# Kernel optimization log

Hardware: AMD Instinct MI355X
Metric: run time of the kernel (lower is better)

## Reference

```python
import jax, jax.numpy as jnp
import numpy as np

B, N, D = 4, 4096, 512          # batch, seq_len, hidden_size
H, DH = 8, 64                    # n_heads, head_dim
M = 512                          # nb_features = 0.125 * seq_len
LN_EPS = 1e-12
KERNEL_EPS = 1e-4


def setup_inputs() -> dict:
    key = jax.random.key(0)
    ks = jax.random.split(key, 12)
    s = 0.02
    return {
        "input_tensor": jax.random.normal(ks[0], (B, N, D), jnp.float32),
        "attention_mask": jnp.zeros((B, 1, 1, N), jnp.float32),  # unused by module
        "Wq": jax.random.normal(ks[1], (D, D), jnp.float32) * s,
        "bq": jnp.zeros((D,), jnp.float32),
        "Wk": jax.random.normal(ks[2], (D, D), jnp.float32) * s,
        "bk": jnp.zeros((D,), jnp.float32),
        "Wv": jax.random.normal(ks[3], (D, D), jnp.float32) * s,
        "bv": jnp.zeros((D,), jnp.float32),
        # gaussian (orthogonal-style) random feature projections [M, DH]
        "proj_q": jax.random.normal(ks[4], (M, DH), jnp.float32),
        "proj_k": jax.random.normal(ks[5], (M, DH), jnp.float32),
        "Wd": jax.random.normal(ks[6], (D, D), jnp.float32) * s,
        "bd": jnp.zeros((D,), jnp.float32),
        "gamma": jnp.ones((D,), jnp.float32),
        "beta": jnp.zeros((D,), jnp.float32),
    }


def _softmax_kernel(data, projection_matrix, is_query):
    # data: [B,H,N,DH], projection_matrix: [M,DH]
    data_normalizer = data.shape[-1] ** (-0.25)
    ratio = projection_matrix.shape[0] ** (-0.5)
    data_dash = jnp.einsum("bhnd,md->bhnm", data_normalizer * data, projection_matrix)
    diag_data = (jnp.sum(data * data, axis=-1) * 0.5 * data_normalizer ** 2)[..., None]
    if is_query:
        stab = jnp.max(data_dash, axis=-1, keepdims=True)
    else:
        stab = jnp.max(data_dash)  # global max, per original code
    return ratio * (jnp.exp(data_dash - diag_data - stab) + KERNEL_EPS)


def _linear_attention(q, k, v):
    # q,k: [B,H,N,M]; v: [B,H,N,DH]
    k_cumsum = jnp.sum(k, axis=-2)                               # [B,H,M]
    d_inv = 1.0 / jnp.einsum("bhnm,bhm->bhn", q, k_cumsum)       # [B,H,N]
    context = jnp.einsum("bhnm,bhne->bhme", k, v)                # [B,H,M,DH]
    return jnp.einsum("bhme,bhnm,bhn->bhne", context, q, d_inv)  # [B,H,N,DH]


def reference(input_tensor, attention_mask, Wq, bq, Wk, bk, Wv, bv,
              proj_q, proj_k, Wd, bd, gamma, beta):
    def heads(x):  # [B,N,D] -> [B,H,N,DH]
        return x.reshape(B, N, H, DH).transpose(0, 2, 1, 3)

    q = heads(input_tensor @ Wq.T + bq)
    k = heads(input_tensor @ Wk.T + bk)
    v = heads(input_tensor @ Wv.T + bv)

    q = _softmax_kernel(q, proj_q, is_query=True)
    k = _softmax_kernel(k, proj_k, is_query=False)

    ctx = _linear_attention(q, k, v)                  # [B,H,N,DH]
    ctx = ctx.transpose(0, 2, 1, 3).reshape(B, N, D)  # merge heads

    hidden = ctx @ Wd.T + bd                          # dropout is identity (eval)
    x = hidden + input_tensor
    mu = jnp.mean(x, axis=-1, keepdims=True)
    var = jnp.mean((x - mu) ** 2, axis=-1, keepdims=True)
    return (x - mu) / jnp.sqrt(var + LN_EPS) * gamma + beta
```

## Files before the change

### kernel.cpp

```cpp
#include <hip/hip_runtime.h>
#include <math.h>

typedef __bf16 bf16;
typedef __bf16 bf16x8 __attribute__((ext_vector_type(8)));
typedef __bf16 bf16x4 __attribute__((ext_vector_type(4)));
typedef float  f32x4  __attribute__((ext_vector_type(4)));

#define NSEQ 4096
#define DMODEL 512
#define DHEAD 64
#define MFEAT 512
#define BHEADS 32
#define ROWS_TOTAL 16384

#define NORMALIZER 0.35355339059327373f
#define DIAG_C 0.0625f
#define KEPS 1e-4f

__device__ __forceinline__ float warpReduceSum(float v) {
#pragma unroll
    for (int off = 32; off > 0; off >>= 1) v += __shfl_xor(v, off);
    return v;
}

__device__ __forceinline__ void atomicMaxF(float* addr, float val) {
    int* ai = (int*)addr;
    int cur = __float_as_int(*addr);
    while (__int_as_float(cur) < val) {
        int prev = atomicCAS(ai, cur, __float_as_int(val));
        if (prev == cur) break;
        cur = prev;
    }
}

__device__ __forceinline__ void gload16(const void* g, void* l) {
    __builtin_amdgcn_global_load_lds((const __attribute__((address_space(1))) void*)g,
                                     (__attribute__((address_space(3))) void*)l, 16, 0, 0);
}

__global__ __launch_bounds__(256)
void prep_convert(const float* __restrict__ x, const float* __restrict__ Wq,
                  const float* __restrict__ Wk, const float* __restrict__ Wv,
                  const float* __restrict__ Wd, const float* __restrict__ pq,
                  const float* __restrict__ bq, const float* __restrict__ bk,
                  const float* __restrict__ bv,
                  bf16* __restrict__ xb, bf16* __restrict__ Wb,
                  bf16* __restrict__ Wdb, bf16* __restrict__ pqb,
                  float* __restrict__ bcat)
{
    size_t i4 = (size_t)blockIdx.x * 256 + threadIdx.x;
    size_t e0 = i4 * 4;
    if (e0 >= 9471488) return;
    const float* src;
    if (e0 < 8388608) {
        src = x + e0;
        float4 v = *(const float4*)src;
        bf16* d = xb + e0;
        d[0] = (bf16)v.x; d[1] = (bf16)v.y; d[2] = (bf16)v.z; d[3] = (bf16)v.w;
    } else if (e0 < 9175040) {
        size_t c = e0 - 8388608; int wsel = (int)(c >> 18); size_t o = c & 262143;
        src = (wsel == 0 ? Wq : wsel == 1 ? Wk : Wv) + o;
        float4 v = *(const float4*)src;
        bf16* d = Wb + c;
        d[0] = (bf16)v.x; d[1] = (bf16)v.y; d[2] = (bf16)v.z; d[3] = (bf16)v.w;
    } else if (e0 < 9437184) {
        size_t c = e0 - 9175040;
        src = Wd + c;
        float4 v = *(const float4*)src;
        bf16* d = Wdb + c;
        d[0] = (bf16)v.x; d[1] = (bf16)v.y; d[2] = (bf16)v.z; d[3] = (bf16)v.w;
    } else if (e0 < 9469952) {
        size_t c = e0 - 9437184;
        src = pq + c;
        float4 v = *(const float4*)src;
        const int feat = (int)(c >> 6), col = (int)(c & 63);
        bf16x4 d4;
        d4[0] = (bf16)v.x; d4[1] = (bf16)v.y; d4[2] = (bf16)v.z; d4[3] = (bf16)v.w;
        const int inrow = (col << 1) ^ ((feat & 7) << 4);
        *(bf16x4*)((char*)pqb + (size_t)feat * 128 + inrow) = d4;
    } else {
        size_t c = e0 - 9469952; int wsel = (int)(c >> 9); size_t o = c & 511;
        src = (wsel == 0 ? bq : wsel == 1 ? bk : bv) + o;
        *(float4*)(bcat + c) = *(const float4*)src;
    }
}

template<int MODE>
__global__ __launch_bounds__(256)
void gemm_mfma(const bf16* __restrict__ A, const bf16* __restrict__ Bw,
               const float* __restrict__ bias, const float* __restrict__ resid,
               bf16* __restrict__ outQ, bf16* __restrict__ outK,
               bf16* __restrict__ outV, float* __restrict__ outF)
{
    __shared__ char As[16384];
    __shared__ char Bs[16384];
    const int tid = threadIdx.x;
    const int w = tid >> 6, l = tid & 63;
    const int wr = w >> 1, wc = w & 1;
    const int row0 = blockIdx.y << 7;
    const int col0 = blockIdx.x << 7;

    f32x4 acc[4][4] = {};
    const char* Ab = (const char*)A + (size_t)row0 * 1024;
    const char* Bb = (const char*)Bw + (size_t)col0 * 1024;

    for (int kt = 0; kt < 8; ++kt) {
        const int k0b = kt << 7;
#pragma unroll
        for (int i = 0; i < 4; ++i) {
            int off = (i << 12) + (tid << 4);
            int g = off ^ ((off >> 3) & 0x70);
            int grow = g >> 7, gcol = g & 127;
            gload16(Ab + (size_t)grow * 1024 + k0b + gcol, As + (i << 12) + (w << 10));
            gload16(Bb + (size_t)grow * 1024 + k0b + gcol, Bs + (i << 12) + (w << 10));
        }
        __syncthreads();
#pragma unroll
        for (int ks = 0; ks < 2; ++ks) {
            bf16x8 af[4], bb[4];
#pragma unroll
            for (int mi = 0; mi < 4; ++mi) {
                int row = (wr << 6) + (mi << 4) + (l & 15);
                int addr = ((row << 7) + (ks << 6) + ((l >> 4) << 4)) ^ ((row & 7) << 4);
                af[mi] = *(const bf16x8*)(As + addr);
            }
#pragma unroll
            for (int nj = 0; nj < 4; ++nj) {
                int row = (wc << 6) + (nj << 4) + (l & 15);
                int addr = ((row << 7) + (ks << 6) + ((l >> 4) << 4)) ^ ((row & 7) << 4);
                bb[nj] = *(const bf16x8*)(Bs + addr);
            }
#pragma unroll
            for (int mi = 0; mi < 4; ++mi)
#pragma unroll
                for (int nj = 0; nj < 4; ++nj)
                    acc[mi][nj] = __builtin_amdgcn_mfma_f32_16x16x32_bf16(af[mi], bb[nj], acc[mi][nj], 0, 0, 0);
        }
        __syncthreads();
    }

    const int subrow = (l >> 4) << 2;
    const int subcol = l & 15;
#pragma unroll
    for (int mi = 0; mi < 4; ++mi) {
#pragma unroll
        for (int nj = 0; nj < 4; ++nj) {
            const int cg = col0 + (wc << 6) + (nj << 4) + subcol;
            const float bi = bias[cg];
            const int rgb = row0 + (wr << 6) + (mi << 4) + subrow;
            if (MODE == 0) {
                if (cg < 512) {
                    const int hh = cg >> 6, ee = cg & 63;
                    const int bb2 = rgb >> 12, n = rgb & 4095;
#pragma unroll
                    for (int r = 0; r < 4; ++r)
                        outQ[((size_t)((bb2 * 8 + hh) * 4096 + n + r)) * 64 + ee] =
                            (bf16)(acc[mi][nj][r] + bi);
                } else if (cg < 1024) {
                    const int eg = cg - 512, hh = eg >> 6, ee = eg & 63;
#pragma unroll
                    for (int r = 0; r < 4; ++r) {
                        const int rg = rgb + r;
                        *(bf16*)((char*)outK + (size_t)rg * 1024 + hh * 128 +
                                 ((ee * 2) ^ ((rg & 7) << 4))) = (bf16)(acc[mi][nj][r] + bi);
                    }
                } else {
                    const int eg = cg - 1024, hh = eg >> 6, ee = eg & 63;
                    const int bb2 = rgb >> 12, n = rgb & 4095;
                    bf16x4 pv;
#pragma unroll
                    for (int r = 0; r < 4; ++r) pv[r] = (bf16)(acc[mi][nj][r] + bi);
                    const int nb = n * 2;
                    size_t byteaddr = (size_t)((bb2 * 8 + hh) * 64 + ee) * 8192
                                    + (size_t)((nb & ~127) | ((nb & 127) ^ ((ee & 7) << 4)));
                    *(bf16x4*)((char*)outV + byteaddr) = pv;
                }
            } else {
#pragma unroll
                for (int r = 0; r < 4; ++r) {
                    const int rg = rgb + r;
                    outF[(size_t)rg * 512 + cg] = acc[mi][nj][r] + bi + resid[(size_t)rg * 512 + cg];
                }
            }
        }
    }
}

__global__ __launch_bounds__(64)
void vsum_kernel(const bf16* __restrict__ Vt, float* __restrict__ vsum)
{
    const int row = blockIdx.x;
    const bf16x8* p = (const bf16x8*)((const char*)Vt + (size_t)row * 8192);
    float s = 0.f;
#pragma unroll
    for (int i = 0; i < 8; ++i) {
        bf16x8 v = p[threadIdx.x + i * 64];
#pragma unroll
        for (int u = 0; u < 8; ++u) s += (float)v[u];
    }
    s = warpReduceSum(s);
    if (threadIdx.x == 0) vsum[row] = s;
}

__global__ __launch_bounds__(256)
void diag_kernel(const bf16* __restrict__ Kb, float* __restrict__ dgk)
{
    const int idx = blockIdx.x * 256 + threadIdx.x;
    const int bh = idx >> 12, n = idx & 4095;
    const int b = bh >> 3, h = bh & 7;
    const char* row = (const char*)Kb + (size_t)(b * 4096 + n) * 1024 + h * 128;
    const int sw = (n & 7) << 4;
    float ss = 0.f;
#pragma unroll
    for (int j = 0; j < 8; ++j) {
        bf16x8 v = *(const bf16x8*)(row + ((j << 4) ^ sw));
#pragma unroll
        for (int u = 0; u < 8; ++u) { float f = (float)v[u]; ss += f * f; }
    }
    dgk[idx] = DIAG_C * ss;
}

__global__ __launch_bounds__(256, 2)
void kside_mfma7(const bf16* __restrict__ Kb, const bf16* __restrict__ Vt,
                 const float* __restrict__ projk, const float* __restrict__ dgk,
                 float* __restrict__ ctxp8, float* __restrict__ esumf8,
                 float* __restrict__ gmax)
{
    __shared__ char K_s[16384];
    __shared__ char V_s[16384];
    __shared__ char E_s[32768];

    const int tid = threadIdx.x;
    const int w = tid >> 6, l = tid & 63;
    const int lq = l & 15, lg = l >> 4;
    const int bh = blockIdx.x;
    const int b = bh >> 3, h = bh & 7;
    const int mw = (blockIdx.y << 8) + (w << 6);
    const int z = blockIdx.z;
    const int swl = (lq & 7) << 4;

    bf16x8 pk[4][2];
#pragma unroll
    for (int mj = 0; mj < 4; ++mj)
#pragma unroll
        for (int ks = 0; ks < 2; ++ks) {
            const int m = mw + (mj << 4) + lq;
            const float* p = projk + (size_t)m * 64 + (ks << 5) + (lg << 3);
            float4 a = *(const float4*)p;
            float4 c = *(const float4*)(p + 4);
            bf16x8 f;
            f[0] = (bf16)(NORMALIZER * a.x); f[1] = (bf16)(NORMALIZER * a.y);
            f[2] = (bf16)(NORMALIZER * a.z); f[3] = (bf16)(NORMALIZER * a.w);
            f[4] = (bf16)(NORMALIZER * c.x); f[5] = (bf16)(NORMALIZER * c.y);
            f[6] = (bf16)(NORMALIZER * c.z); f[7] = (bf16)(NORMALIZER * c.w);
            pk[mj][ks] = f;
        }

    const char* kgb = (const char*)Kb + (size_t)(b * 4096) * 1024 + h * 128;
    const char* vgb = (const char*)Vt + (size_t)bh * 64 * 8192;
    const float* dgb = dgk + (bh << 12) + (z << 9);
    char* tw = E_s + (w << 13);
    const f32x4 Zc = {0.f, 0.f, 0.f, 0.f};

    f32x4 acc2[4][4] = {};
    float esacc[4] = {0.f, 0.f, 0.f, 0.f};
    float lmax = -1e30f;

    {
        const int nc = z << 9;
#pragma unroll
        for (int i = 0; i < 2; ++i) {
            const int lin = tid + (i << 8);
            const int row = lin >> 3, seg = (lin & 7) << 4;
            gload16(kgb + (size_t)(nc + row) * 1024 + seg, K_s + (lin << 4));
            gload16(vgb + (size_t)row * 8192 + (nc << 1) + seg, V_s + (lin << 4));
        }
    }

    int cur = 0;
    for (int c = 0; c < 8; ++c) {
        __syncthreads();
        if (c < 7) {
            const int nn = (z << 9) + ((c + 1) << 6);
#pragma unroll
            for (int i = 0; i < 2; ++i) {
                const int lin = tid + (i << 8);
                const int row = lin >> 3, seg = (lin & 7) << 4;
                gload16(kgb + (size_t)(nn + row) * 1024 + seg,
                        K_s + ((cur ^ 1) << 13) + (lin << 4));
                gload16(vgb + (size_t)row * 8192 + (nn << 1) + seg,
                        V_s + ((cur ^ 1) << 13) + (lin << 4));
            }
        }
        const char* Kc = K_s + (cur << 13);
        const char* Vc = V_s + (cur << 13);

#pragma unroll
        for (int nt = 0; nt < 4; ++nt) {
            const char* kr = Kc + (((nt << 4) + lq) << 7);
            bf16x8 a0 = *(const bf16x8*)(kr + ((lg << 4) ^ swl));
            bf16x8 a1 = *(const bf16x8*)(kr + ((64 + (lg << 4)) ^ swl));
            f32x4 acc1[4];
#pragma unroll
            for (int mj = 0; mj < 4; ++mj) {
                acc1[mj] = __builtin_amdgcn_mfma_f32_16x16x32_bf16(a0, pk[mj][0], Zc, 0, 0, 0);
                acc1[mj] = __builtin_amdgcn_mfma_f32_16x16x32_bf16(a1, pk[mj][1], acc1[mj], 0, 0, 0);
            }
            float4 dv = *(const float4*)(dgb + (c << 6) + (nt << 4) + (lg << 2));
            const float dgr[4] = {dv.x, dv.y, dv.z, dv.w};
#pragma unroll
            for (int mj = 0; mj < 4; ++mj) {
                bf16x4 ev;
#pragma unroll
                for (int r = 0; r < 4; ++r) {
                    const float d = acc1[mj][r];
                    lmax = fmaxf(lmax, d);
                    const float e = __expf(d - dgr[r]);
                    esacc[mj] += e;
                    ev[r] = (bf16)e;
                }
                *(bf16x4*)(tw + (((mj << 4) + lq) << 7) +
                           (((nt << 5) + (lg << 3)) ^ swl)) = ev;
            }
        }
#pragma unroll
        for (int ks2 = 0; ks2 < 2; ++ks2) {
            bf16x8 be[4];
#pragma unroll
            for (int mj = 0; mj < 4; ++mj)
                be[mj] = *(const bf16x8*)(tw + (((mj << 4) + lq) << 7) +
                                          (((ks2 << 6) + (lg << 4)) ^ swl));
#pragma unroll
            for (int et = 0; et < 4; ++et) {
                const int e = (et << 4) + lq;
                bf16x8 av = *(const bf16x8*)(Vc + (e << 7) +
                                             (((ks2 << 6) + (lg << 4)) ^ swl));
#pragma unroll
                for (int mj = 0; mj < 4; ++mj)
                    acc2[et][mj] = __builtin_amdgcn_mfma_f32_16x16x32_bf16(av, be[mj], acc2[et][mj], 0, 0, 0);
            }
        }
        cur ^= 1;
    }

#pragma unroll
    for (int mj = 0; mj < 4; ++mj) {
        float s = esacc[mj];
        s += __shfl_xor(s, 16); s += __shfl_xor(s, 32);
        if (l < 16)
            esumf8[((size_t)z * 32 + bh) * 512 + mw + (mj << 4) + lq] = s;
    }
#pragma unroll
    for (int off = 32; off > 0; off >>= 1) lmax = fmaxf(lmax, __shfl_xor(lmax, off));
    if (l == 0) atomicMaxF(gmax, lmax);

    float* cz = ctxp8 + (size_t)z * (32 * 64 * 512) + (size_t)bh * 64 * 512;
#pragma unroll
    for (int et = 0; et < 4; ++et)
#pragma unroll
        for (int mj = 0; mj < 4; ++mj)
#pragma unroll
            for (int r = 0; r < 4; ++r) {
                const int e = (et << 4) + (lg << 2) + r;
                cz[(size_t)e * 512 + mw + (mj << 4) + lq] = acc2[et][mj][r];
            }
}

__global__ __launch_bounds__(256)
void finalize_ctx(const float* __restrict__ ctxp8, const float* __restrict__ esumf8,
                  bf16* __restrict__ ctxE, float* __restrict__ ctxsum,
                  float* __restrict__ esumsum)
{
    __shared__ float red_s[4][64];
    const int tid = threadIdx.x;
    const int bh = blockIdx.x;
    const int mc = blockIdx.y << 7;
    const int e = tid & 63, ms = tid >> 6;
    const size_t Z = (size_t)32 * 64 * 512;

    const float* cb = ctxp8 + (size_t)bh * 64 * 512 + (size_t)e * 512 + mc + (ms << 5);
    char* obr = (char*)ctxE + ((size_t)bh * 80 + e) * 1024;
    float s = 0.f;
#pragma unroll
    for (int i8 = 0; i8 < 4; ++i8) {
        float acc[8] = {};
#pragma unroll
        for (int zz = 0; zz < 8; ++zz) {
            float4 v0 = *(const float4*)(cb + zz * Z + (i8 << 3));
            float4 v1 = *(const float4*)(cb + zz * Z + (i8 << 3) + 4);
            acc[0] += v0.x; acc[1] += v0.y; acc[2] += v0.z; acc[3] += v0.w;
            acc[4] += v1.x; acc[5] += v1.y; acc[6] += v1.z; acc[7] += v1.w;
        }
        bf16x8 p8;
#pragma unroll
        for (int u = 0; u < 8; ++u) { s += acc[u]; p8[u] = (bf16)acc[u]; }
        const int mloc = mc + (ms << 5) + (i8 << 3);
        *(bf16x8*)(obr + ((mloc << 1) ^ ((e & 7) << 4))) = p8;
    }
    red_s[ms][e] = s;
    __syncthreads();
    if (tid < 64)
        atomicAdd(ctxsum + bh * 64 + tid,
                  red_s[0][tid] + red_s[1][tid] + red_s[2][tid] + red_s[3][tid]);
    if (tid < 128) {
        const int m = mc + tid;
        float ev = 0.f;
#pragma unroll
        for (int zz = 0; zz < 8; ++zz)
            ev += esumf8[((size_t)zz * 32 + bh) * 512 + m];
        bf16* er = ctxE + (size_t)(bh * 80 + 64) * 512;
        er[m] = (bf16)1.0f;
        er[512 + (m ^ 8)] = (bf16)ev;
        float t = warpReduceSum(ev);
        if ((tid & 63) == 0) atomicAdd(esumsum + bh, t);
    }
}

__global__ __launch_bounds__(512, 1)
void qside_mfma4(const bf16* __restrict__ Qb, const bf16* __restrict__ Pq,
                 const bf16* __restrict__ CtxE, const float* __restrict__ vsum,
                 const float* __restrict__ ctxsum, const float* __restrict__ esumsum,
                 const float* __restrict__ gmax, bf16* __restrict__ OutC)
{
    __shared__ char ctx_s[81920];
    __shared__ char pq_s[2][16384];
    __shared__ char T_s[40960];

    const int tid = threadIdx.x;
    const int w = tid >> 6, l = tid & 63;
    const int lq = l & 15, lg = l >> 4;
    const int bh = blockIdx.x;
    const int b = bh >> 3, h = bh & 7;
    const int n0 = blockIdx.y << 9;

    const char* ctxg = (const char*)CtxE + (size_t)bh * 81920;
    const char* pqg  = (const char*)Pq;
#pragma unroll
    for (int i = 0; i < 10; ++i)
        gload16(ctxg + (i << 13) + (tid << 4), ctx_s + (i << 13) + (w << 10));
#pragma unroll
    for (int p = 0; p < 2; ++p)
        gload16(pqg + (p << 13) + (tid << 4), pq_s[0] + (p << 13) + (w << 10));

    const char* qgb = (const char*)Qb + ((size_t)bh * 4096 + n0 + (w << 6)) * 128;
    bf16x8 qa[4][2];
    float diag_l[4];
#pragma unroll
    for (int ni = 0; ni < 4; ++ni) {
        const char* qr = qgb + ((ni << 4) + lq) * 128;
        float ss = 0.f;
#pragma unroll
        for (int kk = 0; kk < 2; ++kk) {
            qa[ni][kk] = *(const bf16x8*)(qr + (kk << 6) + (lg << 4));
#pragma unroll
            for (int u = 0; u < 8; ++u) { float f = (float)qa[ni][kk][u]; ss += f * f; }
        }
        ss += __shfl_xor(ss, 16);
        ss += __shfl_xor(ss, 32);
        diag_l[ni] = DIAG_C * ss;
    }

    f32x4 acc2[4][5] = {};
    float mmax[4] = {-1e30f, -1e30f, -1e30f, -1e30f};
    char* tw = T_s + w * 5120;
    const f32x4 Zc = {0.f, 0.f, 0.f, 0.f};

    __syncthreads();

    for (int ft = 0; ft < 4; ++ft) {
        const int buf = ft & 1;
        if (ft < 3) {
#pragma unroll
            for (int p = 0; p < 2; ++p)
                gload16(pqg + ((ft + 1) << 14) + (p << 13) + (tid << 4),
                        pq_s[buf ^ 1] + (p << 13) + (w << 10));
        }
        const char* pqb = pq_s[buf];
#pragma unroll
        for (int sl = 0; sl < 4; ++sl) {
            f32x4 acc1[2][4];
#pragma unroll
            for (int mi = 0; mi < 2; ++mi) {
                const int fr = (sl << 5) + (mi << 4) + lq;
                bf16x8 pf = *(const bf16x8*)(pqb + fr * 128 +
                              (((lg << 4)) ^ ((lq & 7) << 4)));
#pragma unroll
                for (int ni = 0; ni < 4; ++ni)
                    acc1[mi][ni] = __builtin_amdgcn_mfma_f32_16x16x32_bf16(pf, qa[ni][0], Zc, 0, 0, 0);
            }
#pragma unroll
            for (int mi = 0; mi < 2; ++mi) {
                const int fr = (sl << 5) + (mi << 4) + lq;
                bf16x8 pf = *(const bf16x8*)(pqb + fr * 128 +
                              ((64 + (lg << 4)) ^ ((lq & 7) << 4)));
#pragma unroll
                for (int ni = 0; ni < 4; ++ni)
                    acc1[mi][ni] = __builtin_amdgcn_mfma_f32_16x16x32_bf16(pf, qa[ni][1], acc1[mi][ni], 0, 0, 0);
            }
#pragma unroll
            for (int mi = 0; mi < 2; ++mi)
#pragma unroll
                for (int ni = 0; ni < 4; ++ni) {
                    bf16x4 tv;
#pragma unroll
                    for (int r = 0; r < 4; ++r) {
                        const float qd = acc1[mi][ni][r];
                        mmax[ni] = fmaxf(mmax[ni], qd);
                        tv[r] = (bf16)__expf(NORMALIZER * qd - diag_l[ni]);
                    }
                    *(bf16x4*)(tw + ((ni << 4) + lq) * 80 + (mi << 5) + (lg << 3)) = tv;
                }
            bf16x8 ta[4];
#pragma unroll
            for (int ni = 0; ni < 4; ++ni)
                ta[ni] = *(const bf16x8*)(tw + ((ni << 4) + lq) * 80 + (lg << 4));
#pragma unroll
            for (int nj = 0; nj < 5; ++nj) {
                const int e = (nj << 4) + lq;
                bf16x8 cb = *(const bf16x8*)(ctx_s + e * 1024 +
                              (((ft << 8) + (sl << 6) + (lg << 4)) ^ ((e & 7) << 4)));
#pragma unroll
                for (int ni = 0; ni < 4; ++ni)
                    acc2[ni][nj] = __builtin_amdgcn_mfma_f32_16x16x32_bf16(ta[ni], cb, acc2[ni][nj], 0, 0, 0);
            }
        }
        __syncthreads();
    }

    const float sG = __expf(-gmax[0]);
    const float ess = esumsum[bh];
    bf16* outb = OutC + ((size_t)(b * 4096) + n0 + (w << 6)) * 512 + (h << 6);
#pragma unroll
    for (int ni = 0; ni < 4; ++ni) {
        float mmr = mmax[ni];
        mmr = fmaxf(mmr, __shfl_xor(mmr, 16));
        mmr = fmaxf(mmr, __shfl_xor(mmr, 32));
#pragma unroll
        for (int r = 0; r < 4; ++r) {
            const float mm = __shfl(mmr, (lg << 2) + r);
            const float uT = __shfl(acc2[ni][4][r], (lg << 4));
            const float uE = __shfl(acc2[ni][4][r], (lg << 4) | 1);
            const float cr = __expf(-NORMALIZER * mm);
            const float qsum = cr * uT + KEPS * 512.0f;
            const float D = sG * (cr * uE + KEPS * ess) + KEPS * 4096.0f * qsum;
            const float inv = 1.0f / D;
            const float al = sG * cr * inv;
            const float G1 = sG * KEPS * inv;
            const float G2 = KEPS * qsum * inv;
            const int row = (ni << 4) + (lg << 2) + r;
#pragma unroll
            for (int nj = 0; nj < 4; ++nj) {
                const int e = (nj << 4) + lq;
                float v = al * acc2[ni][nj][r] + G1 * ctxsum[(bh << 6) + e] + G2 * vsum[(bh << 6) + e];
                outb[(size_t)row * 512 + e] = (bf16)v;
            }
        }
    }
}

__global__ __launch_bounds__(256)
void ln_kernel(const float* __restrict__ hid, const float* __restrict__ gamma,
               const float* __restrict__ beta, float* __restrict__ out)
{
    const int row = (blockIdx.x << 2) + (threadIdx.x >> 6);
    const int lane = threadIdx.x & 63;
    const float* x = hid + (size_t)row * DMODEL + (lane << 3);
    float4 a = *(const float4*)x;
    float4 c = *(const float4*)(x + 4);
    float s = a.x + a.y + a.z + a.w + c.x + c.y + c.z + c.w;
    float sq = a.x * a.x + a.y * a.y + a.z * a.z + a.w * a.w +
               c.x * c.x + c.y * c.y + c.z * c.z + c.w * c.w;
    s = warpReduceSum(s);
    sq = warpReduceSum(sq);
    const float mu = s * 0.001953125f;
    const float var = sq * 0.001953125f - mu * mu;
    const float rs = rsqrtf(var + 1e-12f);
    const float4 g1 = *(const float4*)(gamma + (lane << 3));
    const float4 g2 = *(const float4*)(gamma + (lane << 3) + 4);
    const float4 b1 = *(const float4*)(beta + (lane << 3));
    const float4 b2 = *(const float4*)(beta + (lane << 3) + 4);
    float4 o1, o2;
    o1.x = (a.x - mu) * rs * g1.x + b1.x;
    o1.y = (a.y - mu) * rs * g1.y + b1.y;
    o1.z = (a.z - mu) * rs * g1.z + b1.z;
    o1.w = (a.w - mu) * rs * g1.w + b1.w;
    o2.x = (c.x - mu) * rs * g2.x + b2.x;
    o2.y = (c.y - mu) * rs * g2.y + b2.y;
    o2.z = (c.z - mu) * rs * g2.z + b2.z;
    o2.w = (c.w - mu) * rs * g2.w + b2.w;
    *(float4*)(out + (size_t)row * DMODEL + (lane << 3)) = o1;
    *(float4*)(out + (size_t)row * DMODEL + (lane << 3) + 4) = o2;
}

__global__ void init_misc(float* gmax)
{
    if (threadIdx.x == 0 && blockIdx.x == 0) *gmax = -1e30f;
}

extern "C" void kernel_launch(void* const* d_in, const int* in_sizes, int n_in,
                              void* d_out, int out_size, void* d_ws, size_t ws_size,
                              hipStream_t stream)
{
    const float* x     = (const float*)d_in[0];
    const float* Wq    = (const float*)d_in[2];
    const float* bq    = (const float*)d_in[3];
    const float* Wk    = (const float*)d_in[4];
    const float* bk    = (const float*)d_in[5];
    const float* Wv    = (const float*)d_in[6];
    const float* bv    = (const float*)d_in[7];
    const float* projq = (const float*)d_in[8];
    const float* projk = (const float*)d_in[9];
    const float* Wd    = (const float*)d_in[10];
    const float* bd    = (const float*)d_in[11];
    const float* gamma = (const float*)d_in[12];
    const float* beta  = (const float*)d_in[13];

    char* W = (char*)d_ws;
    bf16*  qb16   = (bf16*) (W);
    bf16*  kb16s  = (bf16*) (W + 16777216);
    bf16*  vtb    = (bf16*) (W + 33554432);
    bf16*  xb16   = (bf16*) (W + 50331648);
    float* hidf32 = (float*)(W + 67108864);
    float* ctxp8  = (float*)(W + 67108864);
    float* esumf8 = (float*)(W + 100663296);
    float* dgk    = (float*)(W + 101187584);
    bf16*  Wb16   = (bf16*) (W + 100663296);
    bf16*  Wdb16  = (bf16*) (W + 102236160);
    bf16*  pqb16  = (bf16*) (W + 102760448);
    float* bcat   = (float*)(W + 102825984);
    bf16*  ctxE   = (bf16*) (W + 102832128);
    float* vsumb  = (float*)(W + 105453568);
    float* ctxsum = (float*)(W + 105461760);
    float* esmsm  = (float*)(W + 105469952);
    float* gmaxb  = (float*)(W + 105470080);

    prep_convert<<<9250, 256, 0, stream>>>(x, Wq, Wk, Wv, Wd, projq, bq, bk, bv,
                                           xb16, Wb16, Wdb16, pqb16, bcat);
    hipMemsetAsync(ctxE, 0, 2621440, stream);
    hipMemsetAsync(ctxsum, 0, 8192 + 128, stream);
    init_misc<<<1, 64, 0, stream>>>(gmaxb);

    gemm_mfma<0><<<dim3(12, 128), 256, 0, stream>>>(xb16, Wb16, bcat, nullptr,
                                                    qb16, kb16s, vtb, nullptr);

    diag_kernel<<<512, 256, 0, stream>>>(kb16s, dgk);
    vsum_kernel<<<2048, 64, 0, stream>>>(vtb, vsumb);
    kside_mfma7<<<dim3(32, 2, 8), 256, 0, stream>>>(kb16s, vtb, projk, dgk,
                                                    ctxp8, esumf8, gmaxb);
    finalize_ctx<<<dim3(32, 4), 256, 0, stream>>>(ctxp8, esumf8, ctxE, ctxsum, esmsm);

    qside_mfma4<<<dim3(32, 8), 512, 0, stream>>>(qb16, pqb16, ctxE, vsumb,
                                                 ctxsum, esmsm, gmaxb, xb16);

    gemm_mfma<1><<<dim3(4, 128), 256, 0, stream>>>(xb16, Wdb16, bd, x,
                                                   nullptr, nullptr, nullptr, hidf32);
    ln_kernel<<<4096, 256, 0, stream>>>(hidf32, gamma, beta, (float*)d_out);
}
```

Before: 201.8 us.

## Store K head-major and fuse feature halves into one 512-thread kside block

The QKV GEMM epilogue now writes K in a per-(batch,head) contiguous swizzled layout instead of token-major interleaved heads. This makes K chunk loads one contiguous 8KB block, and diag_kernel addresses rows linearly. The kside kernel now uses 512 threads covering all 512 features in one block, so K and exp tiles are no longer computed twice across blockIdx.y. The whole 64KB V slab for a z-chunk is preloaded once instead of double-buffered, which cuts redundant K loads and projections but raises LDS use to about 144KB and allows only one block per CU.

```diff
diff --git a/kernel.cpp b/kernel.cpp
--- a/kernel.cpp
+++ b/kernel.cpp
@@ -158,11 +158,12 @@
                             (bf16)(acc[mi][nj][r] + bi);
                 } else if (cg < 1024) {
                     const int eg = cg - 512, hh = eg >> 6, ee = eg & 63;
+                    const int bb2 = rgb >> 12;
 #pragma unroll
                     for (int r = 0; r < 4; ++r) {
-                        const int rg = rgb + r;
-                        *(bf16*)((char*)outK + (size_t)rg * 1024 + hh * 128 +
-                                 ((ee * 2) ^ ((rg & 7) << 4))) = (bf16)(acc[mi][nj][r] + bi);
+                        const int nn = (rgb & 4095) + r;
+                        *(bf16*)((char*)outK + ((size_t)(bb2 * 8 + hh) * 4096 + nn) * 128 +
+                                 ((ee * 2) ^ ((nn & 7) << 4))) = (bf16)(acc[mi][nj][r] + bi);
                     }
                 } else {
                     const int eg = cg - 1024, hh = eg >> 6, ee = eg & 63;
@@ -206,9 +207,8 @@
 void diag_kernel(const bf16* __restrict__ Kb, float* __restrict__ dgk)
 {
     const int idx = blockIdx.x * 256 + threadIdx.x;
-    const int bh = idx >> 12, n = idx & 4095;
-    const int b = bh >> 3, h = bh & 7;
-    const char* row = (const char*)Kb + (size_t)(b * 4096 + n) * 1024 + h * 128;
+    const int n = idx & 4095;
+    const char* row = (const char*)Kb + (size_t)idx * 128;
     const int sw = (n & 7) << 4;
     float ss = 0.f;
 #pragma unroll
@@ -220,23 +220,22 @@
     dgk[idx] = DIAG_C * ss;
 }
 
-__global__ __launch_bounds__(256, 2)
-void kside_mfma7(const bf16* __restrict__ Kb, const bf16* __restrict__ Vt,
+__global__ __launch_bounds__(512, 1)
+void kside_mfma8(const bf16* __restrict__ Kb, const bf16* __restrict__ Vt,
                  const float* __restrict__ projk, const float* __restrict__ dgk,
                  float* __restrict__ ctxp8, float* __restrict__ esumf8,
                  float* __restrict__ gmax)
 {
+    __shared__ char V_s[65536];
     __shared__ char K_s[16384];
-    __shared__ char V_s[16384];
-    __shared__ char E_s[32768];
+    __shared__ char E_s[65536];
 
     const int tid = threadIdx.x;
     const int w = tid >> 6, l = tid & 63;
     const int lq = l & 15, lg = l >> 4;
     const int bh = blockIdx.x;
-    const int b = bh >> 3, h = bh & 7;
-    const int mw = (blockIdx.y << 8) + (w << 6);
-    const int z = blockIdx.z;
+    const int z = blockIdx.y;
+    const int mw = w << 6;
     const int swl = (lq & 7) << 4;
 
     bf16x8 pk[4][2];
@@ -256,44 +255,29 @@
             pk[mj][ks] = f;
         }
 
-    const char* kgb = (const char*)Kb + (size_t)(b * 4096) * 1024 + h * 128;
-    const char* vgb = (const char*)Vt + (size_t)bh * 64 * 8192;
+    const char* kgb = (const char*)Kb + (size_t)bh * 524288 + (size_t)(z << 9) * 128;
+    const char* vgb = (const char*)Vt + (size_t)bh * 524288;
     const float* dgb = dgk + (bh << 12) + (z << 9);
     char* tw = E_s + (w << 13);
     const f32x4 Zc = {0.f, 0.f, 0.f, 0.f};
 
+#pragma unroll
+    for (int i = 0; i < 8; ++i)
+        gload16(vgb + (size_t)((i << 3) + w) * 8192 + (z << 10) + ((tid & 63) << 4),
+                V_s + (i << 13) + (tid << 4));
+    gload16(kgb + (tid << 4), K_s + (tid << 4));
+
     f32x4 acc2[4][4] = {};
     float esacc[4] = {0.f, 0.f, 0.f, 0.f};
     float lmax = -1e30f;
 
-    {
-        const int nc = z << 9;
-#pragma unroll
-        for (int i = 0; i < 2; ++i) {
-            const int lin = tid + (i << 8);
-            const int row = lin >> 3, seg = (lin & 7) << 4;
-            gload16(kgb + (size_t)(nc + row) * 1024 + seg, K_s + (lin << 4));
-            gload16(vgb + (size_t)row * 8192 + (nc << 1) + seg, V_s + (lin << 4));
-        }
-    }
-
     int cur = 0;
     for (int c = 0; c < 8; ++c) {
         __syncthreads();
-        if (c < 7) {
-            const int nn = (z << 9) + ((c + 1) << 6);
-#pragma unroll
-            for (int i = 0; i < 2; ++i) {
-                const int lin = tid + (i << 8);
-                const int row = lin >> 3, seg = (lin & 7) << 4;
-                gload16(kgb + (size_t)(nn + row) * 1024 + seg,
-                        K_s + ((cur ^ 1) << 13) + (lin << 4));
-                gload16(vgb + (size_t)row * 8192 + (nn << 1) + seg,
-                        V_s + ((cur ^ 1) << 13) + (lin << 4));
-            }
-        }
+        if (c < 7)
+            gload16(kgb + (size_t)((c + 1) << 13) + (tid << 4),
+                    K_s + ((cur ^ 1) << 13) + (tid << 4));
         const char* Kc = K_s + (cur << 13);
-        const char* Vc = V_s + (cur << 13);
 
 #pragma unroll
         for (int nt = 0; nt < 4; ++nt) {
@@ -333,7 +317,7 @@
 #pragma unroll
             for (int et = 0; et < 4; ++et) {
                 const int e = (et << 4) + lq;
-                bf16x8 av = *(const bf16x8*)(Vc + (e << 7) +
+                bf16x8 av = *(const bf16x8*)(V_s + (e << 10) + (c << 7) +
                                              (((ks2 << 6) + (lg << 4)) ^ swl));
 #pragma unroll
                 for (int mj = 0; mj < 4; ++mj)
@@ -645,8 +629,8 @@
 
     diag_kernel<<<512, 256, 0, stream>>>(kb16s, dgk);
     vsum_kernel<<<2048, 64, 0, stream>>>(vtb, vsumb);
-    kside_mfma7<<<dim3(32, 2, 8), 256, 0, stream>>>(kb16s, vtb, projk, dgk,
-                                                    ctxp8, esumf8, gmaxb);
+    kside_mfma8<<<dim3(32, 8), 512, 0, stream>>>(kb16s, vtb, projk, dgk,
+                                                 ctxp8, esumf8, gmaxb);
     finalize_ctx<<<dim3(32, 4), 256, 0, stream>>>(ctxp8, esumf8, ctxE, ctxsum, esmsm);
 
     qside_mfma4<<<dim3(32, 8), 512, 0, stream>>>(qb16, pqb16, ctxE, vsumb,
```

Result: slower. 214.1 us (+6.1%).
